# Optimization experiments

Hardware: AMD Instinct MI355X
Metric: run time of the kernel (lower is better)

Reference implementation:

```python
import jax, jax.numpy as jnp
import numpy as np

N_NODES = 50000
N_EDGES = 640000
IN_FEAT = 128
OUT_FEAT = 128


def setup_inputs() -> dict:
    key = jax.random.key(0)
    k1, k2, k3 = jax.random.split(key, 3)
    features = jax.random.normal(k1, (N_NODES, IN_FEAT), dtype=jnp.float32)
    edges = jax.random.randint(k2, (2, N_EDGES), 0, N_NODES, dtype=jnp.int64)
    # glorot_uniform for [in_feat, out_feat]
    limit = np.sqrt(6.0 / (IN_FEAT + OUT_FEAT)).astype(np.float32)
    weight = jax.random.uniform(k3, (IN_FEAT, OUT_FEAT), dtype=jnp.float32,
                                minval=-limit, maxval=limit)
    return {"features": features, "edges": edges, "weight": weight}


def reference(features, edges, weight):
    num_nodes = features.shape[0]
    # self representation: [N, out_feat]
    nodes_representation = features @ weight
    # gather source-node features per edge: [E, in_feat]
    neighbour_representations = features[edges[1]]
    # unsorted_segment_mean over destination ids (empty segments -> 0)
    summed = jax.ops.segment_sum(neighbour_representations, edges[0],
                                 num_segments=num_nodes)
    counts = jax.ops.segment_sum(jnp.ones((edges.shape[1],), jnp.float32),
                                 edges[0], num_segments=num_nodes)
    aggregated = jnp.where(counts[:, None] > 0,
                           summed / jnp.maximum(counts, 1.0)[:, None], 0.0)
    aggregated_messages = aggregated @ weight  # [N, out_feat]
    return jax.nn.relu(jnp.concatenate([nodes_representation,
                                        aggregated_messages], axis=-1))
```

## Files before the change

### kernel.cpp

```cpp
#include <hip/hip_runtime.h>

#define N_NODES 50000
#define N_EDGES 640000
#define IN_FEAT 128
#define OUT_FEAT 128
#define CAP 48
#define NBINS 49
#define BINSHIFT 14
#define NSLICE2 32
#define SLICE_CAP 640
#define SHUF_PARTS 16
#define GEMM_BLOCKS 1250
#define FUSED_BLOCKS 1875

typedef unsigned int u32;
typedef unsigned short u16t;
typedef __attribute__((ext_vector_type(8))) short bf16x8;
typedef __attribute__((ext_vector_type(4))) float f32x4;

__device__ __forceinline__ u16t f2bf(float f) {
    union { float f; u32 u; } v; v.f = f;
    u32 r = (v.u + 0x7fffu + ((v.u >> 16) & 1u)) >> 16;
    return (u16t)r;
}
__device__ __forceinline__ float blo(u32 p) {
    union { u32 u; float f; } v; v.u = p << 16; return v.f;
}
__device__ __forceinline__ float bhi(u32 p) {
    union { u32 u; float f; } v; v.u = p & 0xffff0000u; return v.f;
}

__global__ __launch_bounds__(256) void k_prep(const float* __restrict__ weight,
                                              int* __restrict__ cursor,
                                              int* __restrict__ cursor2,
                                              u16t* __restrict__ WbfT) {
    int i = blockIdx.x * 256 + threadIdx.x;
    if (i < 64) cursor[i] = 0;
    int j = i - 64;
    if (j >= 0 && j < NBINS * NSLICE2) cursor2[j] = 0;
    int col = i & 127;
    int k0 = (i >> 7) * 8;
    bf16x8 w;
    #pragma unroll
    for (int jj = 0; jj < 8; ++jj)
        w[jj] = (short)f2bf(weight[(size_t)(k0 + jj) * OUT_FEAT + col]);
    *reinterpret_cast<bf16x8*>(WbfT + (size_t)col * IN_FEAT + k0) = w;
}

__global__ __launch_bounds__(256) void k_fused(const float* __restrict__ feats,
                                               const u16t* __restrict__ WbfT,
                                               const int* __restrict__ edges,
                                               u16t* __restrict__ Ybf,
                                               float* __restrict__ out,
                                               int* __restrict__ cursor,
                                               u32* __restrict__ binbuf) {
    __shared__ float T[16][132];
    __shared__ int sh[192];
    int tid = threadIdx.x;
    int role3 = blockIdx.x % 3;
    if (role3 == 0) {
        int half_id = blockIdx.x / 3;
        int t = half_id * 256 + tid;
        int e0 = t * 4;
        int4 d4 = *reinterpret_cast<const int4*>(edges + e0);
        int4 s4 = *reinterpret_cast<const int4*>(edges + N_EDGES + e0);
        if (tid < 192) sh[tid] = 0;
        __syncthreads();
        int b0 = d4.x >> 10, b1 = d4.y >> 10, b2 = d4.z >> 10, b3 = d4.w >> 10;
        atomicAdd(&sh[b0], 1); atomicAdd(&sh[b1], 1);
        atomicAdd(&sh[b2], 1); atomicAdd(&sh[b3], 1);
        __syncthreads();
        if (tid < 64) {
            int h = sh[tid];
            sh[64 + tid] = h ? atomicAdd(&cursor[tid], h) : 0;
            sh[128 + tid] = 0;
        }
        __syncthreads();
        int o0 = atomicAdd(&sh[128 + b0], 1);
        binbuf[(b0 << BINSHIFT) + sh[64 + b0] + o0] = ((u32)(d4.x & 1023) << 16) | (u32)s4.x;
        int o1 = atomicAdd(&sh[128 + b1], 1);
        binbuf[(b1 << BINSHIFT) + sh[64 + b1] + o1] = ((u32)(d4.y & 1023) << 16) | (u32)s4.y;
        int o2 = atomicAdd(&sh[128 + b2], 1);
        binbuf[(b2 << BINSHIFT) + sh[64 + b2] + o2] = ((u32)(d4.z & 1023) << 16) | (u32)s4.z;
        int o3 = atomicAdd(&sh[128 + b3], 1);
        binbuf[(b3 << BINSHIFT) + sh[64 + b3] + o3] = ((u32)(d4.w & 1023) << 16) | (u32)s4.w;
        return;
    }
    int gemm_id = (blockIdx.x / 3) * 2 + role3 - 1;
    int wid = tid >> 6, lane = tid & 63;
    int ncol0 = wid * 32;
    int krow = lane >> 4;
    int nl = lane & 15;
    int tr = tid >> 4;
    int tc = (tid & 15) * 8;
    bf16x8 bfrag[4][2];
    #pragma unroll
    for (int kb = 0; kb < 4; ++kb) {
        #pragma unroll
        for (int nt = 0; nt < 2; ++nt) {
            bfrag[kb][nt] = *reinterpret_cast<const bf16x8*>(
                WbfT + (size_t)(ncol0 + nt * 16 + nl) * IN_FEAT + kb * 32 + krow * 8);
        }
    }
    for (int mt = gemm_id; mt < N_NODES / 16; mt += GEMM_BLOCKS) {
        const float* arow = feats + (size_t)(mt * 16 + nl) * IN_FEAT + krow * 8;
        f32x4 acc0 = {0.f, 0.f, 0.f, 0.f};
        f32x4 acc1 = {0.f, 0.f, 0.f, 0.f};
        #pragma unroll
        for (int kb = 0; kb < 4; ++kb) {
            float4 a0 = *reinterpret_cast<const float4*>(arow + kb * 32);
            float4 a1 = *reinterpret_cast<const float4*>(arow + kb * 32 + 4);
            bf16x8 a;
            a[0] = (short)f2bf(a0.x); a[1] = (short)f2bf(a0.y);
            a[2] = (short)f2bf(a0.z); a[3] = (short)f2bf(a0.w);
            a[4] = (short)f2bf(a1.x); a[5] = (short)f2bf(a1.y);
            a[6] = (short)f2bf(a1.z); a[7] = (short)f2bf(a1.w);
            acc0 = __builtin_amdgcn_mfma_f32_16x16x32_bf16(a, bfrag[kb][0], acc0, 0, 0, 0);
            acc1 = __builtin_amdgcn_mfma_f32_16x16x32_bf16(a, bfrag[kb][1], acc1, 0, 0, 0);
        }
        __syncthreads();
        #pragma unroll
        for (int r = 0; r < 4; ++r) {
            T[krow * 4 + r][ncol0 + nl]      = acc0[r];
            T[krow * 4 + r][ncol0 + 16 + nl] = acc1[r];
        }
        __syncthreads();
        int node = mt * 16 + tr;
        float4 v0 = *reinterpret_cast<const float4*>(&T[tr][tc]);
        float4 v1 = *reinterpret_cast<const float4*>(&T[tr][tc + 4]);
        bf16x8 yb;
        yb[0] = (short)f2bf(v0.x); yb[1] = (short)f2bf(v0.y);
        yb[2] = (short)f2bf(v0.z); yb[3] = (short)f2bf(v0.w);
        yb[4] = (short)f2bf(v1.x); yb[5] = (short)f2bf(v1.y);
        yb[6] = (short)f2bf(v1.z); yb[7] = (short)f2bf(v1.w);
        *reinterpret_cast<bf16x8*>(Ybf + (size_t)node * OUT_FEAT + tc) = yb;
        float4 r0, r1;
        r0.x = fmaxf(v0.x, 0.f); r0.y = fmaxf(v0.y, 0.f);
        r0.z = fmaxf(v0.z, 0.f); r0.w = fmaxf(v0.w, 0.f);
        r1.x = fmaxf(v1.x, 0.f); r1.y = fmaxf(v1.y, 0.f);
        r1.z = fmaxf(v1.z, 0.f); r1.w = fmaxf(v1.w, 0.f);
        float* orow = out + (size_t)node * (2 * OUT_FEAT) + tc;
        *reinterpret_cast<float4*>(orow)     = r0;
        *reinterpret_cast<float4*>(orow + 4) = r1;
    }
}

__global__ __launch_bounds__(256) void k_shuf(const int* __restrict__ cursor,
                                              const u32* __restrict__ binbuf,
                                              int* __restrict__ cursor2,
                                              u32* __restrict__ binbuf2) {
    __shared__ int hist[NSLICE2], base[NSLICE2], cur[NSLICE2];
    int tid = threadIdx.x;
    int bin = blockIdx.x / SHUF_PARTS, part = blockIdx.x % SHUF_PARTS;
    int nb = cursor[bin];
    if (nb > (1 << BINSHIFT)) nb = 1 << BINSHIFT;
    int s = nb * part / SHUF_PARTS, e = nb * (part + 1) / SHUF_PARTS;
    const u32* bb = binbuf + ((size_t)bin << BINSHIFT);
    if (tid < NSLICE2) hist[tid] = 0;
    __syncthreads();
    for (int j = s + tid; j < e; j += 256) {
        int sl = (int)((bb[j] >> 21) & 31u);
        atomicAdd(&hist[sl], 1);
    }
    __syncthreads();
    if (tid < NSLICE2) {
        int h = hist[tid];
        base[tid] = h ? atomicAdd(&cursor2[bin * NSLICE2 + tid], h) : 0;
        cur[tid] = 0;
    }
    __syncthreads();
    for (int j = s + tid; j < e; j += 256) {
        u32 p = bb[j];
        int sl = (int)((p >> 21) & 31u);
        int o = atomicAdd(&cur[sl], 1);
        int pos = base[sl] + o;
        if (pos < SLICE_CAP)
            binbuf2[(size_t)(bin * NSLICE2 + sl) * SLICE_CAP + pos] = p;
    }
}

__global__ __launch_bounds__(256) void k_acc(const u16t* __restrict__ Ybf,
                                             const int* __restrict__ cursor2,
                                             const u32* __restrict__ binbuf2,
                                             float* __restrict__ out) {
    __shared__ u16t lbkt[NSLICE2 * CAP];
    __shared__ int lcnt[NSLICE2];
    int tid = threadIdx.x;
    int bin = blockIdx.x >> 5, slice = blockIdx.x & 31;
    if (tid < NSLICE2) lcnt[tid] = 0;
    __syncthreads();
    int nb = cursor2[bin * NSLICE2 + slice];
    if (nb > SLICE_CAP) nb = SLICE_CAP;
    const u32* bb2 = binbuf2 + (size_t)(bin * NSLICE2 + slice) * SLICE_CAP;
    for (int j = tid; j < nb; j += 256) {
        u32 p = bb2[j];
        int da = (int)((p >> 16) & 31u);
        int pos = atomicAdd(&lcnt[da], 1);
        if (pos < CAP) lbkt[da * CAP + pos] = (u16t)(p & 0xffffu);
    }
    __syncthreads();
    int wid = tid >> 6, lane = tid & 63;
    int half = lane >> 5, l5 = lane & 31;
    for (int i = 0; i < 8; ++i) {
        int r = wid * 8 + i;
        int node = (bin << 10) + (slice << 5) + r;
        if (node >= N_NODES) break;
        int deg = lcnt[r];
        int m = (deg < CAP) ? deg : CAP;
        const u16t* b = &lbkt[r * CAP];
        float s0 = 0.f, s1 = 0.f, s2 = 0.f, s3 = 0.f;
        int j = half;
        for (; j + 7 <= m; j += 8) {
            int sa = (int)b[j], sb = (int)b[j + 2], sc = (int)b[j + 4], sd = (int)b[j + 6];
            uint2 pa = *reinterpret_cast<const uint2*>(Ybf + (size_t)sa * OUT_FEAT + 4 * l5);
            uint2 pb = *reinterpret_cast<const uint2*>(Ybf + (size_t)sb * OUT_FEAT + 4 * l5);
            uint2 pc = *reinterpret_cast<const uint2*>(Ybf + (size_t)sc * OUT_FEAT + 4 * l5);
            uint2 pd = *reinterpret_cast<const uint2*>(Ybf + (size_t)sd * OUT_FEAT + 4 * l5);
            s0 += (blo(pa.x) + blo(pb.x)) + (blo(pc.x) + blo(pd.x));
            s1 += (bhi(pa.x) + bhi(pb.x)) + (bhi(pc.x) + bhi(pd.x));
            s2 += (blo(pa.y) + blo(pb.y)) + (blo(pc.y) + blo(pd.y));
            s3 += (bhi(pa.y) + bhi(pb.y)) + (bhi(pc.y) + bhi(pd.y));
        }
        for (; j < m; j += 2) {
            int sa = (int)b[j];
            uint2 pa = *reinterpret_cast<const uint2*>(Ybf + (size_t)sa * OUT_FEAT + 4 * l5);
            s0 += blo(pa.x); s1 += bhi(pa.x);
            s2 += blo(pa.y); s3 += bhi(pa.y);
        }
        s0 += __shfl_xor(s0, 32); s1 += __shfl_xor(s1, 32);
        s2 += __shfl_xor(s2, 32); s3 += __shfl_xor(s3, 32);
        if (half == 0) {
            float inv = (deg > 0) ? 1.f / (float)deg : 0.f;
            float4 v;
            v.x = fmaxf(s0 * inv, 0.f); v.y = fmaxf(s1 * inv, 0.f);
            v.z = fmaxf(s2 * inv, 0.f); v.w = fmaxf(s3 * inv, 0.f);
            *reinterpret_cast<float4*>(out + (size_t)node * (2 * OUT_FEAT) + OUT_FEAT + 4 * l5) = v;
        }
    }
}

extern "C" void kernel_launch(void* const* d_in, const int* in_sizes, int n_in,
                              void* d_out, int out_size, void* d_ws, size_t ws_size,
                              hipStream_t stream) {
    const float* feats  = (const float*)d_in[0];
    const int*   edges  = (const int*)d_in[1];
    const float* weight = (const float*)d_in[2];
    float* out = (float*)d_out;

    u16t* Ybf     = (u16t*)d_ws;
    int*  cursor  = (int*)(Ybf + (size_t)N_NODES * OUT_FEAT);
    int*  cursor2 = cursor + 64;
    u16t* WbfT    = (u16t*)(cursor2 + NBINS * NSLICE2);
    u32*  binbuf  = (u32*)(WbfT + IN_FEAT * OUT_FEAT);
    u32*  binbuf2 = binbuf + ((size_t)64 << BINSHIFT);

    hipLaunchKernelGGL(k_prep,  dim3(8), dim3(256), 0, stream,
                       weight, cursor, cursor2, WbfT);
    hipLaunchKernelGGL(k_fused, dim3(FUSED_BLOCKS), dim3(256), 0, stream,
                       feats, WbfT, edges, Ybf, out, cursor, binbuf);
    hipLaunchKernelGGL(k_shuf,  dim3(NBINS * SHUF_PARTS), dim3(256), 0, stream,
                       cursor, binbuf, cursor2, binbuf2);
    hipLaunchKernelGGL(k_acc,   dim3(NBINS * NSLICE2), dim3(256), 0, stream,
                       Ybf, cursor2, binbuf2, out);
}
```

Baseline: 66.73 us.

## Replace global atomic cursors with per-block fixed-capacity bins and drop prep kernel

Edge binning now writes each block's per-bin edges into its own fixed-capacity segment with a per-block count, instead of reserving space through global atomic cursors. The shuffle and accumulate stages follow the same per-part segment layout. The weight bf16 conversion moves into the GEMM blocks, so the separate prep/zeroing kernel and one launch are removed. The trade-offs are that each GEMM block re-reads and converts the weights with strided loads, and the per-segment caps (56, 64) silently drop edges whenever a segment overflows.

```diff
diff --git a/kernel.cpp b/kernel.cpp
--- a/kernel.cpp
+++ b/kernel.cpp
@@ -6,10 +6,11 @@
 #define OUT_FEAT 128
 #define CAP 48
 #define NBINS 49
-#define BINSHIFT 14
+#define NBLK 625
+#define CAP2 56
 #define NSLICE2 32
-#define SLICE_CAP 640
-#define SHUF_PARTS 16
+#define NPART 16
+#define CAP3 64
 #define GEMM_BLOCKS 1250
 #define FUSED_BLOCKS 1875
 
@@ -30,60 +31,42 @@
     union { u32 u; float f; } v; v.u = p & 0xffff0000u; return v.f;
 }
 
-__global__ __launch_bounds__(256) void k_prep(const float* __restrict__ weight,
-                                              int* __restrict__ cursor,
-                                              int* __restrict__ cursor2,
-                                              u16t* __restrict__ WbfT) {
-    int i = blockIdx.x * 256 + threadIdx.x;
-    if (i < 64) cursor[i] = 0;
-    int j = i - 64;
-    if (j >= 0 && j < NBINS * NSLICE2) cursor2[j] = 0;
-    int col = i & 127;
-    int k0 = (i >> 7) * 8;
-    bf16x8 w;
-    #pragma unroll
-    for (int jj = 0; jj < 8; ++jj)
-        w[jj] = (short)f2bf(weight[(size_t)(k0 + jj) * OUT_FEAT + col]);
-    *reinterpret_cast<bf16x8*>(WbfT + (size_t)col * IN_FEAT + k0) = w;
-}
-
 __global__ __launch_bounds__(256) void k_fused(const float* __restrict__ feats,
-                                               const u16t* __restrict__ WbfT,
+                                               const float* __restrict__ weight,
                                                const int* __restrict__ edges,
                                                u16t* __restrict__ Ybf,
                                                float* __restrict__ out,
-                                               int* __restrict__ cursor,
-                                               u32* __restrict__ binbuf) {
+                                               int* __restrict__ cnt1,
+                                               u32* __restrict__ binbufD) {
     __shared__ float T[16][132];
-    __shared__ int sh[192];
+    __shared__ int cur[64];
     int tid = threadIdx.x;
     int role3 = blockIdx.x % 3;
     if (role3 == 0) {
-        int half_id = blockIdx.x / 3;
-        int t = half_id * 256 + tid;
-        int e0 = t * 4;
+        int blk = blockIdx.x / 3;
+        int e0 = (blk * 256 + tid) * 4;
         int4 d4 = *reinterpret_cast<const int4*>(edges + e0);
         int4 s4 = *reinterpret_cast<const int4*>(edges + N_EDGES + e0);
-        if (tid < 192) sh[tid] = 0;
+        if (tid < 64) cur[tid] = 0;
         __syncthreads();
         int b0 = d4.x >> 10, b1 = d4.y >> 10, b2 = d4.z >> 10, b3 = d4.w >> 10;
-        atomicAdd(&sh[b0], 1); atomicAdd(&sh[b1], 1);
-        atomicAdd(&sh[b2], 1); atomicAdd(&sh[b3], 1);
-        __syncthreads();
-        if (tid < 64) {
-            int h = sh[tid];
-            sh[64 + tid] = h ? atomicAdd(&cursor[tid], h) : 0;
-            sh[128 + tid] = 0;
-        }
-        __syncthreads();
-        int o0 = atomicAdd(&sh[128 + b0], 1);
-        binbuf[(b0 << BINSHIFT) + sh[64 + b0] + o0] = ((u32)(d4.x & 1023) << 16) | (u32)s4.x;
-        int o1 = atomicAdd(&sh[128 + b1], 1);
-        binbuf[(b1 << BINSHIFT) + sh[64 + b1] + o1] = ((u32)(d4.y & 1023) << 16) | (u32)s4.y;
-        int o2 = atomicAdd(&sh[128 + b2], 1);
-        binbuf[(b2 << BINSHIFT) + sh[64 + b2] + o2] = ((u32)(d4.z & 1023) << 16) | (u32)s4.z;
-        int o3 = atomicAdd(&sh[128 + b3], 1);
-        binbuf[(b3 << BINSHIFT) + sh[64 + b3] + o3] = ((u32)(d4.w & 1023) << 16) | (u32)s4.w;
+        int o0 = atomicAdd(&cur[b0], 1);
+        if (o0 < CAP2) binbufD[(size_t)(b0 * NBLK + blk) * CAP2 + o0] =
+            ((u32)(d4.x & 1023) << 16) | (u32)s4.x;
+        int o1 = atomicAdd(&cur[b1], 1);
+        if (o1 < CAP2) binbufD[(size_t)(b1 * NBLK + blk) * CAP2 + o1] =
+            ((u32)(d4.y & 1023) << 16) | (u32)s4.y;
+        int o2 = atomicAdd(&cur[b2], 1);
+        if (o2 < CAP2) binbufD[(size_t)(b2 * NBLK + blk) * CAP2 + o2] =
+            ((u32)(d4.z & 1023) << 16) | (u32)s4.z;
+        int o3 = atomicAdd(&cur[b3], 1);
+        if (o3 < CAP2) binbufD[(size_t)(b3 * NBLK + blk) * CAP2 + o3] =
+            ((u32)(d4.w & 1023) << 16) | (u32)s4.w;
+        __syncthreads();
+        if (tid < NBINS) {
+            int c = cur[tid];
+            cnt1[tid * NBLK + blk] = (c < CAP2) ? c : CAP2;
+        }
         return;
     }
     int gemm_id = (blockIdx.x / 3) * 2 + role3 - 1;
@@ -98,8 +81,13 @@
     for (int kb = 0; kb < 4; ++kb) {
         #pragma unroll
         for (int nt = 0; nt < 2; ++nt) {
-            bfrag[kb][nt] = *reinterpret_cast<const bf16x8*>(
-                WbfT + (size_t)(ncol0 + nt * 16 + nl) * IN_FEAT + kb * 32 + krow * 8);
+            bf16x8 b;
+            #pragma unroll
+            for (int j = 0; j < 8; ++j) {
+                int k = kb * 32 + krow * 8 + j;
+                b[j] = (short)f2bf(weight[(size_t)k * OUT_FEAT + ncol0 + nt * 16 + nl]);
+            }
+            bfrag[kb][nt] = b;
         }
     }
     for (int mt = gemm_id; mt < N_NODES / 16; mt += GEMM_BLOCKS) {
@@ -145,42 +133,36 @@
     }
 }
 
-__global__ __launch_bounds__(256) void k_shuf(const int* __restrict__ cursor,
-                                              const u32* __restrict__ binbuf,
-                                              int* __restrict__ cursor2,
+__global__ __launch_bounds__(256) void k_shuf(const int* __restrict__ cnt1,
+                                              const u32* __restrict__ binbufD,
+                                              int* __restrict__ cnt2,
                                               u32* __restrict__ binbuf2) {
-    __shared__ int hist[NSLICE2], base[NSLICE2], cur[NSLICE2];
+    __shared__ int cur2[NSLICE2];
     int tid = threadIdx.x;
-    int bin = blockIdx.x / SHUF_PARTS, part = blockIdx.x % SHUF_PARTS;
-    int nb = cursor[bin];
-    if (nb > (1 << BINSHIFT)) nb = 1 << BINSHIFT;
-    int s = nb * part / SHUF_PARTS, e = nb * (part + 1) / SHUF_PARTS;
-    const u32* bb = binbuf + ((size_t)bin << BINSHIFT);
-    if (tid < NSLICE2) hist[tid] = 0;
-    __syncthreads();
-    for (int j = s + tid; j < e; j += 256) {
-        int sl = (int)((bb[j] >> 21) & 31u);
-        atomicAdd(&hist[sl], 1);
+    int bin = blockIdx.x >> 4, part = blockIdx.x & 15;
+    if (tid < NSLICE2) cur2[tid] = 0;
+    __syncthreads();
+    int s = (NBLK * part) >> 4, e = (NBLK * (part + 1)) >> 4;
+    for (int blk = s + (tid >> 4); blk < e; blk += 16) {
+        int n = cnt1[bin * NBLK + blk];
+        const u32* seg = binbufD + (size_t)(bin * NBLK + blk) * CAP2;
+        for (int j = tid & 15; j < n; j += 16) {
+            u32 p = seg[j];
+            int sl = (int)((p >> 21) & 31u);
+            int o = atomicAdd(&cur2[sl], 1);
+            if (o < CAP3)
+                binbuf2[(size_t)((bin * NSLICE2 + sl) * NPART + part) * CAP3 + o] = p;
+        }
     }
     __syncthreads();
     if (tid < NSLICE2) {
-        int h = hist[tid];
-        base[tid] = h ? atomicAdd(&cursor2[bin * NSLICE2 + tid], h) : 0;
-        cur[tid] = 0;
-    }
-    __syncthreads();
-    for (int j = s + tid; j < e; j += 256) {
-        u32 p = bb[j];
-        int sl = (int)((p >> 21) & 31u);
-        int o = atomicAdd(&cur[sl], 1);
-        int pos = base[sl] + o;
-        if (pos < SLICE_CAP)
-            binbuf2[(size_t)(bin * NSLICE2 + sl) * SLICE_CAP + pos] = p;
+        int c = cur2[tid];
+        cnt2[(bin * NSLICE2 + tid) * NPART + part] = (c < CAP3) ? c : CAP3;
     }
 }
 
 __global__ __launch_bounds__(256) void k_acc(const u16t* __restrict__ Ybf,
-                                             const int* __restrict__ cursor2,
+                                             const int* __restrict__ cnt2,
                                              const u32* __restrict__ binbuf2,
                                              float* __restrict__ out) {
     __shared__ u16t lbkt[NSLICE2 * CAP];
@@ -189,14 +171,17 @@
     int bin = blockIdx.x >> 5, slice = blockIdx.x & 31;
     if (tid < NSLICE2) lcnt[tid] = 0;
     __syncthreads();
-    int nb = cursor2[bin * NSLICE2 + slice];
-    if (nb > SLICE_CAP) nb = SLICE_CAP;
-    const u32* bb2 = binbuf2 + (size_t)(bin * NSLICE2 + slice) * SLICE_CAP;
-    for (int j = tid; j < nb; j += 256) {
-        u32 p = bb2[j];
-        int da = (int)((p >> 16) & 31u);
-        int pos = atomicAdd(&lcnt[da], 1);
-        if (pos < CAP) lbkt[da * CAP + pos] = (u16t)(p & 0xffffu);
+    int base2 = (bin * NSLICE2 + slice) * NPART;
+    {
+        int p = tid >> 4;
+        int n = cnt2[base2 + p];
+        const u32* seg = binbuf2 + (size_t)(base2 + p) * CAP3;
+        for (int j = tid & 15; j < n; j += 16) {
+            u32 pk = seg[j];
+            int da = (int)((pk >> 16) & 31u);
+            int pos = atomicAdd(&lcnt[da], 1);
+            if (pos < CAP) lbkt[da * CAP + pos] = (u16t)(pk & 0xffffu);
+        }
     }
     __syncthreads();
     int wid = tid >> 6, lane = tid & 63;
@@ -248,18 +233,15 @@
     float* out = (float*)d_out;
 
     u16t* Ybf     = (u16t*)d_ws;
-    int*  cursor  = (int*)(Ybf + (size_t)N_NODES * OUT_FEAT);
-    int*  cursor2 = cursor + 64;
-    u16t* WbfT    = (u16t*)(cursor2 + NBINS * NSLICE2);
-    u32*  binbuf  = (u32*)(WbfT + IN_FEAT * OUT_FEAT);
-    u32*  binbuf2 = binbuf + ((size_t)64 << BINSHIFT);
-
-    hipLaunchKernelGGL(k_prep,  dim3(8), dim3(256), 0, stream,
-                       weight, cursor, cursor2, WbfT);
+    int*  cnt1    = (int*)(Ybf + (size_t)N_NODES * OUT_FEAT);
+    u32*  binbufD = (u32*)(cnt1 + NBINS * NBLK);
+    int*  cnt2    = (int*)(binbufD + (size_t)NBINS * NBLK * CAP2);
+    u32*  binbuf2 = (u32*)(cnt2 + NBINS * NSLICE2 * NPART);
+
     hipLaunchKernelGGL(k_fused, dim3(FUSED_BLOCKS), dim3(256), 0, stream,
-                       feats, WbfT, edges, Ybf, out, cursor, binbuf);
-    hipLaunchKernelGGL(k_shuf,  dim3(NBINS * SHUF_PARTS), dim3(256), 0, stream,
-                       cursor, binbuf, cursor2, binbuf2);
+                       feats, weight, edges, Ybf, out, cnt1, binbufD);
+    hipLaunchKernelGGL(k_shuf,  dim3(NBINS * NPART), dim3(256), 0, stream,
+                       cnt1, binbufD, cnt2, binbuf2);
     hipLaunchKernelGGL(k_acc,   dim3(NBINS * NSLICE2), dim3(256), 0, stream,
-                       Ybf, cursor2, binbuf2, out);
-}
+                       Ybf, cnt2, binbuf2, out);
+}
```

Result: faster. 61.79 us, median of 2 (-7.4%).
